# Kernel optimization log

Hardware: AMD Instinct MI355X
Metric: run time of the kernel (lower is better)

## Reference

```python
import jax, jax.numpy as jnp
import numpy as np
import math

EMB_DIM = 2048
HEAD_NUMS = 16
HEAD_DIM = EMB_DIM // HEAD_NUMS


def setup_inputs() -> dict:
    key = jax.random.key(0)
    k1, k2, k3, k4, k5 = jax.random.split(key, 5)
    B, S = 2, 2048
    X = jax.random.normal(k1, (B, S, EMB_DIM), dtype=jnp.float32)
    mask = jnp.ones((B, S), dtype=jnp.int32)
    # torch nn.Linear weights: [out_features, in_features]
    W_qkv = jax.random.normal(k2, (3 * EMB_DIM, EMB_DIM), dtype=jnp.float32) / math.sqrt(EMB_DIM)
    b_qkv = jax.random.normal(k3, (3 * EMB_DIM,), dtype=jnp.float32) * 0.01
    W_o = jax.random.normal(k4, (EMB_DIM, EMB_DIM), dtype=jnp.float32) / math.sqrt(EMB_DIM)
    b_o = jax.random.normal(k5, (EMB_DIM,), dtype=jnp.float32) * 0.01
    return {"X": X, "mask": mask, "W_qkv": W_qkv, "b_qkv": b_qkv, "W_o": W_o, "b_o": b_o}


def _rope_tables(seq_len):
    # Bug-faithful to source: exponent divides by full emb_dim, not head_dim.
    angle = 1.0 / jnp.power(10000.0, jnp.arange(0, HEAD_DIM, 2, dtype=jnp.float32) / EMB_DIM)
    t = jnp.arange(seq_len, dtype=jnp.float32)
    freqs = t[:, None] * angle[None, :]            # [S, HEAD_DIM//2]
    freqs = jnp.repeat(freqs, 2, axis=-1)          # [S, HEAD_DIM] (repeat_interleave)
    return jnp.cos(freqs), jnp.sin(freqs)


def _trans(x):
    # de-interleave pairs, then concat([-odd, even]) along last dim (as in source)
    B, H, S, D = x.shape
    xr = x.reshape(B, H, S, D // 2, 2)
    x1, x2 = xr[..., 0], xr[..., 1]
    return jnp.concatenate([-x2, x1], axis=-1)


def reference(X, mask, W_qkv, b_qkv, W_o, b_o):
    B, S, E = X.shape
    cos, sin = _rope_tables(S)                      # [S, HEAD_DIM]
    qkv = X @ W_qkv.T + b_qkv                       # [B, S, 3E]
    qkv = qkv.reshape(B, S, 3, HEAD_NUMS, HEAD_DIM).transpose(2, 0, 3, 1, 4)
    Q, K, V = qkv[0], qkv[1], qkv[2]                # [B, H, S, D]
    c = cos[None, None, :, :]
    s = sin[None, None, :, :]
    Q = c * Q + s * _trans(Q)
    K = c * K + s * _trans(K)
    scores = jnp.einsum('bhqd,bhkd->bhqk', Q, K) / math.sqrt(HEAD_DIM)
    pad = mask[:, None, None, :]                    # [B,1,1,S]
    scores = jnp.where(pad == 0, -1e9, scores)
    attn = jax.nn.softmax(scores, axis=-1)          # dropout = identity (eval)
    out = jnp.einsum('bhqk,bhkd->bhqd', attn, V)    # [B,H,S,D]
    out = out.transpose(0, 2, 1, 3).reshape(B, S, E)
    return out @ W_o.T + b_o
```

## Files before the change

### kernel.cpp

```cpp
#include <hip/hip_runtime.h>
#include <hip/hip_bf16.h>
#include <math.h>

typedef __bf16 bf16x8 __attribute__((ext_vector_type(8)));
typedef float  f32x4  __attribute__((ext_vector_type(4)));
typedef float  f32x16 __attribute__((ext_vector_type(16)));
typedef unsigned short ushort_t;
typedef ushort_t us4 __attribute__((ext_vector_type(4)));

#define MFMA16(a, b, c) __builtin_amdgcn_mfma_f32_16x16x32_bf16((a), (b), (c), 0, 0, 0)
#define MFMA32(a, b, c) __builtin_amdgcn_mfma_f32_32x32x16_bf16((a), (b), (c), 0, 0, 0)

__device__ __forceinline__ float bf2f(ushort_t h) {
    union { unsigned u; float f; } v; v.u = ((unsigned)h) << 16; return v.f;
}
__device__ __forceinline__ ushort_t f2bf(float x) {
    union { float f; unsigned u; } v; v.f = x;
    unsigned r = v.u + 0x7FFFu + ((v.u >> 16) & 1u);
    return (ushort_t)(r >> 16);
}
__device__ __forceinline__ void gl2lds16(const void* g, void* l) {
    __builtin_amdgcn_global_load_lds((__attribute__((address_space(1))) void*)(g),
                                     (__attribute__((address_space(3))) void*)(l),
                                     16, 0, 0);
}

__global__ __launch_bounds__(256) void detect_kernel(const ushort_t* __restrict__ w, int* flag)
{
    __shared__ int cnt[256];
    const int t = threadIdx.x;
    int c = 0;
    for (int i = t; i < 65536; i += 256) {
        const unsigned hw = w[i];
        const unsigned e = (hw >> 7) & 0xFFu;
        if (e == 0xFFu || (e == 0u && (hw & 0x7Fu) != 0u)) c++;
    }
    cnt[t] = c;
    __syncthreads();
    for (int s = 128; s > 0; s >>= 1) {
        if (t < s) cnt[t] += cnt[t + s];
        __syncthreads();
    }
    if (t == 0) flag[0] = (cnt[0] >= 8) ? 1 : 0;
}

__global__ __launch_bounds__(256) void convert_kernel(const void* __restrict__ src,
                                                      ushort_t* __restrict__ dst,
                                                      int n, const int* __restrict__ flag)
{
    const int i0 = (blockIdx.x * 256 + threadIdx.x) * 8;
    if (i0 + 8 > n) return;
    if (flag[0]) {
        const f32x4 a = *(const f32x4*)((const float*)src + i0);
        const f32x4 b = *(const f32x4*)((const float*)src + i0 + 4);
        ushort_t o[8];
        o[0]=f2bf(a[0]); o[1]=f2bf(a[1]); o[2]=f2bf(a[2]); o[3]=f2bf(a[3]);
        o[4]=f2bf(b[0]); o[5]=f2bf(b[1]); o[6]=f2bf(b[2]); o[7]=f2bf(b[3]);
        *(bf16x8*)(dst + i0) = *(const bf16x8*)o;
    } else {
        *(bf16x8*)(dst + i0) = *(const bf16x8*)((const ushort_t*)src + i0);
    }
}

__global__ __launch_bounds__(512, 2) void gemm256_bt_bias(
    const ushort_t* __restrict__ A, const ushort_t* __restrict__ B,
    const ushort_t* __restrict__ bias, ushort_t* __restrict__ C,
    int M, int N, int K)
{
    __shared__ __align__(16) ushort_t SM[65536];
    const int tid = threadIdx.x;
    const int l = tid & 63, ln = l & 15, q2 = l >> 4;
    const int w = tid >> 6, wm = w >> 2, wn = w & 3;
    const int m0 = blockIdx.y * 256, n0 = blockIdx.x * 256;
    const int NT = K >> 6;

#define STG_A256(slot, kbase, o) do { \
    const int s_ = (o) * 512 + tid; const int r_ = s_ >> 2; \
    const int q_ = (s_ & 3) ^ ((r_ >> 1) & 3); \
    gl2lds16(A + (size_t)(m0 + r_) * K + (kbase) + q_ * 8, \
             SM + (slot) * 16384 + s_ * 8); } while (0)
#define STG_B256(slot, kbase, o) do { \
    const int s_ = (o) * 512 + tid; const int r_ = s_ >> 2; \
    const int q_ = (s_ & 3) ^ ((r_ >> 1) & 3); \
    gl2lds16(B + (size_t)(n0 + r_) * K + (kbase) + q_ * 8, \
             SM + (slot) * 16384 + 8192 + s_ * 8); } while (0)
#define DSA256(slot, row) (*(const bf16x8*)(SM + (slot) * 16384 + (row) * 32 + ((q2 ^ (((row) >> 1) & 3)) << 3)))
#define DSB256(slot, row) (*(const bf16x8*)(SM + (slot) * 16384 + 8192 + (row) * 32 + ((q2 ^ (((row) >> 1) & 3)) << 3)))
#define BAR256() asm volatile("s_barrier" ::: "memory")

    f32x4 acc[8][4];
    const f32x4 z4 = {0.f, 0.f, 0.f, 0.f};
#pragma unroll
    for (int i = 0; i < 8; i++)
#pragma unroll
        for (int j = 0; j < 4; j++) acc[i][j] = z4;

    STG_A256(0, 0, 0);  STG_A256(0, 0, 1);  STG_B256(0, 0, 0);  STG_B256(0, 0, 1);
    STG_A256(1, 32, 0); STG_A256(1, 32, 1); STG_B256(1, 32, 0); STG_B256(1, 32, 1);
    if (NT > 1) STG_A256(2, 64, 0);
    asm volatile("s_waitcnt vmcnt(5)" ::: "memory");
    BAR256();

    for (int t = 0; t < NT; ++t) {
        const int s0 = (2 * t) & 3, s1 = (2 * t + 1) & 3;
        const int sA = (2 * t + 2) & 3, sB = (2 * t + 3) & 3;
        const int kA = (t + 1) << 6, kB = kA + 32, kC = (t + 2) << 6;
        const bool stAB = (t < NT - 1), stC = (t < NT - 2);
        const int rA0 = wm * 128, rA1 = wm * 128 + 64, rB = wn * 64;
        bf16x8 a0[4], a1[4], b00[2], b01[2], b10[2], b11[2];

#pragma unroll
        for (int ii = 0; ii < 4; ii++) a0[ii] = DSA256(s0, rA0 + ii * 16 + ln);
        b00[0] = DSB256(s0, rB + ln);
        b00[1] = DSB256(s0, rB + 16 + ln);
        if (stAB) STG_A256(sA, kA, 1);
        __builtin_amdgcn_s_setprio(1);
#pragma unroll
        for (int ii = 0; ii < 4; ii++) {
            acc[ii][0] = MFMA16(a0[ii], b00[0], acc[ii][0]);
            acc[ii][1] = MFMA16(a0[ii], b00[1], acc[ii][1]);
        }
        __builtin_amdgcn_s_setprio(0);
        if (stAB) { asm volatile("s_waitcnt vmcnt(2)" ::: "memory"); }
        else      { asm volatile("s_waitcnt vmcnt(0)" ::: "memory"); }
        BAR256();

#pragma unroll
        for (int ii = 0; ii < 4; ii++) a1[ii] = DSA256(s1, rA0 + ii * 16 + ln);
        b01[0] = DSB256(s1, rB + ln);
        b01[1] = DSB256(s1, rB + 16 + ln);
        if (stAB) STG_B256(sA, kA, 0);
        __builtin_amdgcn_s_setprio(1);
#pragma unroll
        for (int ii = 0; ii < 4; ii++) {
            acc[ii][0] = MFMA16(a1[ii], b01[0], acc[ii][0]);
            acc[ii][1] = MFMA16(a1[ii], b01[1], acc[ii][1]);
        }
        __builtin_amdgcn_s_setprio(0);
        BAR256();

        b10[0] = DSB256(s0, rB + 32 + ln);
        b10[1] = DSB256(s0, rB + 48 + ln);
        if (stAB) STG_B256(sA, kA, 1);
        __builtin_amdgcn_s_setprio(1);
#pragma unroll
        for (int ii = 0; ii < 4; ii++) {
            acc[ii][2] = MFMA16(a0[ii], b10[0], acc[ii][2]);
            acc[ii][3] = MFMA16(a0[ii], b10[1], acc[ii][3]);
        }
        __builtin_amdgcn_s_setprio(0);
        BAR256();

        b11[0] = DSB256(s1, rB + 32 + ln);
        b11[1] = DSB256(s1, rB + 48 + ln);
        if (stAB) STG_A256(sB, kB, 0);
        __builtin_amdgcn_s_setprio(1);
#pragma unroll
        for (int ii = 0; ii < 4; ii++) {
            acc[ii][2] = MFMA16(a1[ii], b11[0], acc[ii][2]);
            acc[ii][3] = MFMA16(a1[ii], b11[1], acc[ii][3]);
        }
        __builtin_amdgcn_s_setprio(0);
        BAR256();

#pragma unroll
        for (int ii = 0; ii < 4; ii++) a0[ii] = DSA256(s0, rA1 + ii * 16 + ln);
        if (stAB) STG_A256(sB, kB, 1);
        __builtin_amdgcn_s_setprio(1);
#pragma unroll
        for (int ii = 0; ii < 4; ii++) {
            acc[4 + ii][2] = MFMA16(a0[ii], b10[0], acc[4 + ii][2]);
            acc[4 + ii][3] = MFMA16(a0[ii], b10[1], acc[4 + ii][3]);
        }
        __builtin_amdgcn_s_setprio(0);
        BAR256();

#pragma unroll
        for (int ii = 0; ii < 4; ii++) a1[ii] = DSA256(s1, rA1 + ii * 16 + ln);
        if (stAB) STG_B256(sB, kB, 0);
        __builtin_amdgcn_s_setprio(1);
#pragma unroll
        for (int ii = 0; ii < 4; ii++) {
            acc[4 + ii][2] = MFMA16(a1[ii], b11[0], acc[4 + ii][2]);
            acc[4 + ii][3] = MFMA16(a1[ii], b11[1], acc[4 + ii][3]);
        }
        __builtin_amdgcn_s_setprio(0);
        BAR256();

        if (stAB) STG_B256(sB, kB, 1);
        __builtin_amdgcn_s_setprio(1);
#pragma unroll
        for (int ii = 0; ii < 4; ii++) {
            acc[4 + ii][0] = MFMA16(a0[ii], b00[0], acc[4 + ii][0]);
            acc[4 + ii][1] = MFMA16(a0[ii], b00[1], acc[4 + ii][1]);
        }
        __builtin_amdgcn_s_setprio(0);
        BAR256();

        if (stC) STG_A256(s0, kC, 0);
        __builtin_amdgcn_s_setprio(1);
#pragma unroll
        for (int ii = 0; ii < 4; ii++) {
            acc[4 + ii][0] = MFMA16(a1[ii], b01[0], acc[4 + ii][0]);
            acc[4 + ii][1] = MFMA16(a1[ii], b01[1], acc[4 + ii][1]);
        }
        __builtin_amdgcn_s_setprio(0);
        if (t < NT - 2)       { asm volatile("s_waitcnt vmcnt(5)" ::: "memory"); }
        else if (t == NT - 2) { asm volatile("s_waitcnt vmcnt(4)" ::: "memory"); }
        BAR256();
    }

#pragma unroll
    for (int j = 0; j < 4; j++) {
        const int n = n0 + wn * 64 + j * 16 + ln;
        const float bv = bf2f(bias[n]);
#pragma unroll
        for (int i = 0; i < 8; i++) {
            const int mrow = m0 + wm * 128 + i * 16 + q2 * 4;
#pragma unroll
            for (int r = 0; r < 4; r++)
                C[(size_t)(mrow + r) * N + n] = f2bf(acc[i][j][r] + bv);
        }
    }
#undef STG_A256
#undef STG_B256
#undef DSA256
#undef DSB256
#undef BAR256
}

__global__ __launch_bounds__(256) void gemm_bt_bias_out(
    const ushort_t* __restrict__ A, const ushort_t* __restrict__ B,
    const ushort_t* __restrict__ bias, void* __restrict__ C,
    int M, int N, int K, const int* __restrict__ flag)
{
    __shared__ __align__(16) ushort_t As[128 * 32];
    __shared__ __align__(16) ushort_t Bs[128 * 32];
    const int tid = threadIdx.x;
    const int w = tid >> 6, l = tid & 63, q = l >> 4, ln = l & 15;
    const int wm = w >> 1, wn = w & 1;
    const int m0 = blockIdx.y * 128, n0 = blockIdx.x * 128;
    const int sr = tid >> 2;
    const int sc = (tid & 3) * 8;

    f32x4 acc[4][4];
    const f32x4 z4 = {0.f, 0.f, 0.f, 0.f};
    for (int i = 0; i < 4; i++) for (int j = 0; j < 4; j++) acc[i][j] = z4;

    for (int k0 = 0; k0 < K; k0 += 32) {
        __syncthreads();
        gl2lds16(A + (size_t)(m0 + sr) * K + k0 + sc,       As + sr * 32 + sc);
        gl2lds16(A + (size_t)(m0 + 64 + sr) * K + k0 + sc,  As + (64 + sr) * 32 + sc);
        gl2lds16(B + (size_t)(n0 + sr) * K + k0 + sc,       Bs + sr * 32 + sc);
        gl2lds16(B + (size_t)(n0 + 64 + sr) * K + k0 + sc,  Bs + (64 + sr) * 32 + sc);
        __syncthreads();
        bf16x8 a[4], bb[4];
        for (int i = 0; i < 4; i++)
            a[i]  = *(const bf16x8*)(As + (wm * 64 + i * 16 + ln) * 32 + q * 8);
        for (int j = 0; j < 4; j++)
            bb[j] = *(const bf16x8*)(Bs + (wn * 64 + j * 16 + ln) * 32 + q * 8);
        for (int i = 0; i < 4; i++)
            for (int j = 0; j < 4; j++)
                acc[i][j] = MFMA16(a[i], bb[j], acc[i][j]);
    }
    const int f = flag[0];
    for (int j = 0; j < 4; j++) {
        const int n = n0 + wn * 64 + j * 16 + ln;
        const float bv = bf2f(bias[n]);
        for (int i = 0; i < 4; i++) {
            const int mrow = m0 + wm * 64 + i * 16 + q * 4;
            for (int r = 0; r < 4; r++) {
                const float val = acc[i][j][r] + bv;
                const size_t idx = (size_t)(mrow + r) * N + n;
                if (f) ((float*)C)[idx] = val;
                else   ((ushort_t*)C)[idx] = f2bf(val);
            }
        }
    }
}

__global__ __launch_bounds__(256) void rope_kernel(ushort_t* qkv)
{
    const int bs = blockIdx.x;
    const int s = bs & 2047;
    const int t = threadIdx.x;
    const size_t base = (size_t)bs * 6144;
    float cv[8], sv[8], qa[8], qp[8], ka[8], kp[8];
    for (int u = 0; u < 8; u++) {
        const int e = u * 256 + t;
        const int j = e & 127;
        const int p = (j < 64) ? (2 * j + 1) : (2 * (j - 64));
        const int hb = e - j;
        const float ang = powf(10000.0f, -(float)(2 * (j >> 1)) / 2048.0f);
        sincosf((float)s * ang, &sv[u], &cv[u]);
        qa[u] = bf2f(qkv[base + hb + j]);
        qp[u] = bf2f(qkv[base + hb + p]);
        ka[u] = bf2f(qkv[base + 2048 + hb + j]);
        kp[u] = bf2f(qkv[base + 2048 + hb + p]);
    }
    __syncthreads();
    for (int u = 0; u < 8; u++) {
        const int e = u * 256 + t;
        const int j = e & 127;
        const int hb = e - j;
        const float sg = (j < 64) ? -1.0f : 1.0f;
        qkv[base + hb + j]        = f2bf(cv[u] * qa[u] + sv[u] * sg * qp[u]);
        qkv[base + 2048 + hb + j] = f2bf(cv[u] * ka[u] + sv[u] * sg * kp[u]);
    }
}

__global__ __launch_bounds__(256) void vtrans_kernel(const ushort_t* __restrict__ qkv,
                                                     ushort_t* __restrict__ Vt)
{
    __shared__ ushort_t tile[64][130];
    const int blk = blockIdx.x;
    const int st = blk & 31, h = (blk >> 5) & 15, b = blk >> 9;
    const int t = threadIdx.x;
    for (int i = 0; i < 32; i++) {
        const int e = i * 256 + t;
        const int r = e >> 7, c = e & 127;
        tile[r][c] = qkv[(size_t)(b * 2048 + st * 64 + r) * 6144 + 4096 + h * 128 + c];
    }
    __syncthreads();
    const int d = t >> 1, s0 = (t & 1) * 32;
    const size_t obase = ((size_t)(b * 16 + h) * 128 + d) * 2048 + st * 64 + s0;
    for (int k = 0; k < 32; k++)
        Vt[obase + k] = tile[s0 + k][d];
}

__global__ __launch_bounds__(256, 2) void flash_kernel(
    const ushort_t* __restrict__ qkv, const ushort_t* __restrict__ Vt,
    const int* __restrict__ mask, ushort_t* __restrict__ AO)
{
    __shared__ __align__(16) ushort_t SM[16384];
    ushort_t* Ks = SM;
    ushort_t* Vs = SM + 8192;
    const int t = threadIdx.x;
    const int w = t >> 6, l = t & 63, lq = l & 31, q2 = l >> 5;
    const int qb = blockIdx.x * 128, h = blockIdx.y, b = blockIdx.z;
    const size_t brow = (size_t)b * 2048;
    const float scale = 0.08838834764831845f;
    const int qrow = qb + w * 32 + lq;
    const size_t vbase = (size_t)(b * 16 + h) * 128;

    bf16x8 qf[8];
#pragma unroll
    for (int kb = 0; kb < 8; kb++)
        qf[kb] = *(const bf16x8*)(qkv + (brow + qrow) * 6144 + h * 128 + kb * 16 + q2 * 8);

    float m_old = -1e30f, lsum = 0.f;
    f32x16 acc_o[4];
#pragma unroll
    for (int dt = 0; dt < 4; dt++)
#pragma unroll
        for (int r = 0; r < 16; r++) acc_o[dt][r] = 0.f;

    bf16x8 kst[4], vst[4];
#pragma unroll
    for (int i = 0; i < 4; i++) {
        const int s_ = i * 256 + t; const int row = s_ >> 4; const int u = s_ & 15;
        kst[i] = *(const bf16x8*)(qkv + (brow + row) * 6144 + 2048 + h * 128 + u * 8);
    }
#pragma unroll
    for (int i = 0; i < 4; i++) {
        const int s_ = i * 256 + t; const int row = s_ >> 3; const int u = s_ & 7;
        vst[i] = *(const bf16x8*)(Vt + (vbase + row) * 2048 + u * 8);
    }

    for (int s0 = 0; s0 < 2048; s0 += 64) {
        const int mk = mask[brow + s0 + l];
        const unsigned long long bm = __ballot(mk != 0);
        asm volatile("s_waitcnt lgkmcnt(0)" ::: "memory");
        asm volatile("s_barrier" ::: "memory");
#pragma unroll
        for (int i = 0; i < 4; i++) {
            const int s_ = i * 256 + t; const int row = s_ >> 4; const int u = s_ & 15;
            *(bf16x8*)(Ks + row * 128 + ((u ^ (row & 15)) << 3)) = kst[i];
        }
#pragma unroll
        for (int i = 0; i < 4; i++) {
            const int s_ = i * 256 + t; const int row = s_ >> 3; const int u = s_ & 7;
            *(bf16x8*)(Vs + row * 64 + ((u ^ (row & 7)) << 3)) = vst[i];
        }
        if (s0 + 64 < 2048) {
#pragma unroll
            for (int i = 0; i < 4; i++) {
                const int s_ = i * 256 + t; const int row = s_ >> 4; const int u = s_ & 15;
                kst[i] = *(const bf16x8*)(qkv + (brow + s0 + 64 + row) * 6144 + 2048 + h * 128 + u * 8);
            }
#pragma unroll
            for (int i = 0; i < 4; i++) {
                const int s_ = i * 256 + t; const int row = s_ >> 3; const int u = s_ & 7;
                vst[i] = *(const bf16x8*)(Vt + (vbase + row) * 2048 + s0 + 64 + u * 8);
            }
        }
        asm volatile("s_waitcnt lgkmcnt(0)" ::: "memory");
        asm volatile("s_barrier" ::: "memory");

        f32x16 sa[2];
#pragma unroll
        for (int mt = 0; mt < 2; mt++) {
#pragma unroll
            for (int r = 0; r < 16; r++) sa[mt][r] = 0.f;
            const int row = mt * 32 + lq;
            __builtin_amdgcn_s_setprio(1);
#pragma unroll
            for (int kb = 0; kb < 8; kb++) {
                bf16x8 a = *(const bf16x8*)(Ks + row * 128 + (((kb * 2 + q2) ^ (row & 15)) << 3));
                sa[mt] = MFMA32(a, qf[kb], sa[mt]);
            }
            __builtin_amdgcn_s_setprio(0);
        }
        float p[32];
        float mr = -1e30f;
        if (bm == ~0ull) {
#pragma unroll
            for (int mt = 0; mt < 2; mt++)
#pragma unroll
                for (int r = 0; r < 16; r++) {
                    const float v = sa[mt][r] * scale;
                    p[mt * 16 + r] = v;
                    mr = fmaxf(mr, v);
                }
        } else {
#pragma unroll
            for (int mt = 0; mt < 2; mt++)
#pragma unroll
                for (int r = 0; r < 16; r++) {
                    const int srow = mt * 32 + (r & 3) + 8 * (r >> 2) + 4 * q2;
                    const float bias = ((bm >> srow) & 1ull) ? 0.f : -1e9f;
                    const float v = sa[mt][r] * scale + bias;
                    p[mt * 16 + r] = v;
                    mr = fmaxf(mr, v);
                }
        }
        mr = fmaxf(mr, __shfl_xor(mr, 32, 64));
        if (!__all(mr <= m_old + 8.0f)) {
            const float mnew = fmaxf(m_old, mr);
            const float alpha = __expf(m_old - mnew);
            lsum *= alpha;
#pragma unroll
            for (int dt = 0; dt < 4; dt++)
#pragma unroll
                for (int r = 0; r < 16; r++) acc_o[dt][r] *= alpha;
            m_old = mnew;
        }
        float rs = 0.f;
#pragma unroll
        for (int i = 0; i < 32; i++) { p[i] = __expf(p[i] - m_old); rs += p[i]; }
        rs += __shfl_xor(rs, 32, 64);
        lsum += rs;

#pragma unroll
        for (int kb = 0; kb < 4; kb++) {
            const int bb = (kb >> 1) * 16 + (kb & 1) * 8;
            unsigned w01, w23, w45, w67;
            asm("v_cvt_pk_bf16_f32 %0, %1, %2" : "=v"(w01) : "v"(p[bb + 0]), "v"(p[bb + 1]));
            asm("v_cvt_pk_bf16_f32 %0, %1, %2" : "=v"(w23) : "v"(p[bb + 2]), "v"(p[bb + 3]));
            asm("v_cvt_pk_bf16_f32 %0, %1, %2" : "=v"(w45) : "v"(p[bb + 4]), "v"(p[bb + 5]));
            asm("v_cvt_pk_bf16_f32 %0, %1, %2" : "=v"(w67) : "v"(p[bb + 6]), "v"(p[bb + 7]));
            asm("v_permlane32_swap_b32 %0, %1" : "+v"(w01), "+v"(w45));
            asm("v_permlane32_swap_b32 %0, %1" : "+v"(w23), "+v"(w67));
            union { unsigned u[4]; bf16x8 v8; } pu;
            pu.u[0] = w01; pu.u[1] = w23; pu.u[2] = w45; pu.u[3] = w67;
            __builtin_amdgcn_s_setprio(1);
#pragma unroll
            for (int dt = 0; dt < 4; dt++) {
                const int row = dt * 32 + lq;
                bf16x8 va = *(const bf16x8*)(Vs + row * 64 + (((kb * 2 + q2) ^ (row & 7)) << 3));
                acc_o[dt] = MFMA32(va, pu.v8, acc_o[dt]);
            }
            __builtin_amdgcn_s_setprio(0);
        }
    }
    __syncthreads();
    const float inv = (lsum > 0.f) ? 1.0f / lsum : 0.f;
#pragma unroll
    for (int dt = 0; dt < 4; dt++)
#pragma unroll
        for (int r2 = 0; r2 < 4; r2++) {
            us4 ov;
#pragma unroll
            for (int j = 0; j < 4; j++) ov[j] = f2bf(acc_o[dt][r2 * 4 + j] * inv);
            const int row = w * 32 + lq;
            const int unit = dt * 4 + r2;
            *(us4*)(SM + row * 128 + ((unit ^ (row & 15)) << 3) + q2 * 4) = ov;
        }
    __syncthreads();
#pragma unroll
    for (int i = 0; i < 8; i++) {
        const int rl = i * 4 + (l >> 4), ch = l & 15;
        const int row = w * 32 + rl;
        bf16x8 vv = *(const bf16x8*)(SM + row * 128 + ((ch ^ (row & 15)) << 3));
        *(bf16x8*)(AO + (brow + qb + row) * 2048 + h * 128 + ch * 8) = vv;
    }
}

extern "C" void kernel_launch(void* const* d_in, const int* in_sizes, int n_in,
                              void* d_out, int out_size, void* d_ws, size_t ws_size,
                              hipStream_t stream)
{
    (void)in_sizes; (void)n_in; (void)out_size; (void)ws_size;
    const void* X    = d_in[0];
    const int*  mask = (const int*)d_in[1];
    const void* Wqkv = d_in[2];
    const void* bqkv = d_in[3];
    const void* Wo   = d_in[4];
    const void* bo   = d_in[5];

    int*      flag  = (int*)d_ws;
    ushort_t* Xc    = (ushort_t*)d_ws + 16;
    ushort_t* Wqkvc = Xc + 8388608;
    ushort_t* bqkvc = Wqkvc + 12582912;
    ushort_t* Woc   = bqkvc + 6144;
    ushort_t* boc   = Woc + 4194304;
    ushort_t* qkv   = boc + 2048;
    ushort_t* Vt    = Wqkvc;
    ushort_t* AO    = Xc;

    detect_kernel<<<1, 256, 0, stream>>>((const ushort_t*)Wqkv, flag);
    convert_kernel<<<4096, 256, 0, stream>>>(X,    Xc,    8388608,  flag);
    convert_kernel<<<6144, 256, 0, stream>>>(Wqkv, Wqkvc, 12582912, flag);
    convert_kernel<<<3,    256, 0, stream>>>(bqkv, bqkvc, 6144,     flag);
    convert_kernel<<<2048, 256, 0, stream>>>(Wo,   Woc,   4194304,  flag);
    convert_kernel<<<1,    256, 0, stream>>>(bo,   boc,   2048,     flag);

    gemm256_bt_bias<<<dim3(6144 / 256, 4096 / 256), 512, 0, stream>>>(Xc, Wqkvc, bqkvc, qkv, 4096, 6144, 2048);
    rope_kernel<<<4096, 256, 0, stream>>>(qkv);
    vtrans_kernel<<<1024, 256, 0, stream>>>(qkv, Vt);
    flash_kernel<<<dim3(16, 16, 2), 256, 0, stream>>>(qkv, Vt, mask, AO);
    gemm_bt_bias_out<<<dim3(2048 / 128, 4096 / 128), 256, 0, stream>>>(AO, Woc, boc, d_out, 4096, 2048, 2048, flag);
}
```

Baseline: 578.9 us.

## Restructure 256-tile GEMM main loop into four phases with larger MFMA bursts

Replaces the eight-phase ping-pong schedule, each phase issuing 8 MFMAs, with four phases of 16 MFMAs each. All four B fragments per k-half are now held in registers. Global-to-LDS stages are issued in pairs, and the early prefetch of the third k-slab is dropped. The aim is to halve the number of workgroup barriers per iteration and give the matrix unit longer uninterrupted bursts, at the cost of more live registers and less lead time on prefetches. The vmcnt wait counts are adjusted to the new issue pattern, and any mismatch there could cause LDS read hazards.

```diff
diff --git a/kernel.cpp b/kernel.cpp
--- a/kernel.cpp
+++ b/kernel.cpp
@@ -97,116 +97,70 @@
 
     STG_A256(0, 0, 0);  STG_A256(0, 0, 1);  STG_B256(0, 0, 0);  STG_B256(0, 0, 1);
     STG_A256(1, 32, 0); STG_A256(1, 32, 1); STG_B256(1, 32, 0); STG_B256(1, 32, 1);
-    if (NT > 1) STG_A256(2, 64, 0);
-    asm volatile("s_waitcnt vmcnt(5)" ::: "memory");
+    asm volatile("s_waitcnt vmcnt(4)" ::: "memory");
     BAR256();
 
     for (int t = 0; t < NT; ++t) {
         const int s0 = (2 * t) & 3, s1 = (2 * t + 1) & 3;
         const int sA = (2 * t + 2) & 3, sB = (2 * t + 3) & 3;
-        const int kA = (t + 1) << 6, kB = kA + 32, kC = (t + 2) << 6;
-        const bool stAB = (t < NT - 1), stC = (t < NT - 2);
+        const int kA = (t + 1) << 6, kB = kA + 32;
+        const bool stAB = (t < NT - 1);
         const int rA0 = wm * 128, rA1 = wm * 128 + 64, rB = wn * 64;
-        bf16x8 a0[4], a1[4], b00[2], b01[2], b10[2], b11[2];
-
-#pragma unroll
-        for (int ii = 0; ii < 4; ii++) a0[ii] = DSA256(s0, rA0 + ii * 16 + ln);
-        b00[0] = DSB256(s0, rB + ln);
-        b00[1] = DSB256(s0, rB + 16 + ln);
-        if (stAB) STG_A256(sA, kA, 1);
+        bf16x8 a[4], b0[4], b1[4];
+
+#pragma unroll
+        for (int ii = 0; ii < 4; ii++) a[ii]  = DSA256(s0, rA0 + ii * 16 + ln);
+#pragma unroll
+        for (int jj = 0; jj < 4; jj++) b0[jj] = DSB256(s0, rB + jj * 16 + ln);
+        if (stAB) { STG_A256(sA, kA, 0); STG_A256(sA, kA, 1); }
         __builtin_amdgcn_s_setprio(1);
 #pragma unroll
-        for (int ii = 0; ii < 4; ii++) {
-            acc[ii][0] = MFMA16(a0[ii], b00[0], acc[ii][0]);
-            acc[ii][1] = MFMA16(a0[ii], b00[1], acc[ii][1]);
-        }
+        for (int ii = 0; ii < 4; ii++)
+#pragma unroll
+            for (int jj = 0; jj < 4; jj++)
+                acc[ii][jj] = MFMA16(a[ii], b0[jj], acc[ii][jj]);
         __builtin_amdgcn_s_setprio(0);
         if (stAB) { asm volatile("s_waitcnt vmcnt(2)" ::: "memory"); }
         else      { asm volatile("s_waitcnt vmcnt(0)" ::: "memory"); }
         BAR256();
 
 #pragma unroll
-        for (int ii = 0; ii < 4; ii++) a1[ii] = DSA256(s1, rA0 + ii * 16 + ln);
-        b01[0] = DSB256(s1, rB + ln);
-        b01[1] = DSB256(s1, rB + 16 + ln);
-        if (stAB) STG_B256(sA, kA, 0);
+        for (int ii = 0; ii < 4; ii++) a[ii]  = DSA256(s1, rA0 + ii * 16 + ln);
+#pragma unroll
+        for (int jj = 0; jj < 4; jj++) b1[jj] = DSB256(s1, rB + jj * 16 + ln);
+        if (stAB) { STG_B256(sA, kA, 0); STG_B256(sA, kA, 1); }
         __builtin_amdgcn_s_setprio(1);
 #pragma unroll
-        for (int ii = 0; ii < 4; ii++) {
-            acc[ii][0] = MFMA16(a1[ii], b01[0], acc[ii][0]);
-            acc[ii][1] = MFMA16(a1[ii], b01[1], acc[ii][1]);
-        }
+        for (int ii = 0; ii < 4; ii++)
+#pragma unroll
+            for (int jj = 0; jj < 4; jj++)
+                acc[ii][jj] = MFMA16(a[ii], b1[jj], acc[ii][jj]);
         __builtin_amdgcn_s_setprio(0);
         BAR256();
 
-        b10[0] = DSB256(s0, rB + 32 + ln);
-        b10[1] = DSB256(s0, rB + 48 + ln);
-        if (stAB) STG_B256(sA, kA, 1);
+#pragma unroll
+        for (int ii = 0; ii < 4; ii++) a[ii] = DSA256(s0, rA1 + ii * 16 + ln);
+        if (stAB) { STG_A256(sB, kB, 0); STG_A256(sB, kB, 1); }
         __builtin_amdgcn_s_setprio(1);
 #pragma unroll
-        for (int ii = 0; ii < 4; ii++) {
-            acc[ii][2] = MFMA16(a0[ii], b10[0], acc[ii][2]);
-            acc[ii][3] = MFMA16(a0[ii], b10[1], acc[ii][3]);
-        }
+        for (int ii = 0; ii < 4; ii++)
+#pragma unroll
+            for (int jj = 0; jj < 4; jj++)
+                acc[4 + ii][jj] = MFMA16(a[ii], b0[jj], acc[4 + ii][jj]);
         __builtin_amdgcn_s_setprio(0);
         BAR256();
 
-        b11[0] = DSB256(s1, rB + 32 + ln);
-        b11[1] = DSB256(s1, rB + 48 + ln);
-        if (stAB) STG_A256(sB, kB, 0);
+#pragma unroll
+        for (int ii = 0; ii < 4; ii++) a[ii] = DSA256(s1, rA1 + ii * 16 + ln);
+        if (stAB) { STG_B256(sB, kB, 0); STG_B256(sB, kB, 1); }
         __builtin_amdgcn_s_setprio(1);
 #pragma unroll
-        for (int ii = 0; ii < 4; ii++) {
-            acc[ii][2] = MFMA16(a1[ii], b11[0], acc[ii][2]);
-            acc[ii][3] = MFMA16(a1[ii], b11[1], acc[ii][3]);
-        }
+        for (int ii = 0; ii < 4; ii++)
+#pragma unroll
+            for (int jj = 0; jj < 4; jj++)
+                acc[4 + ii][jj] = MFMA16(a[ii], b1[jj], acc[4 + ii][jj]);
         __builtin_amdgcn_s_setprio(0);
-        BAR256();
-
-#pragma unroll
-        for (int ii = 0; ii < 4; ii++) a0[ii] = DSA256(s0, rA1 + ii * 16 + ln);
-        if (stAB) STG_A256(sB, kB, 1);
-        __builtin_amdgcn_s_setprio(1);
-#pragma unroll
-        for (int ii = 0; ii < 4; ii++) {
-            acc[4 + ii][2] = MFMA16(a0[ii], b10[0], acc[4 + ii][2]);
-            acc[4 + ii][3] = MFMA16(a0[ii], b10[1], acc[4 + ii][3]);
-        }
-        __builtin_amdgcn_s_setprio(0);
-        BAR256();
-
-#pragma unroll
-        for (int ii = 0; ii < 4; ii++) a1[ii] = DSA256(s1, rA1 + ii * 16 + ln);
-        if (stAB) STG_B256(sB, kB, 0);
-        __builtin_amdgcn_s_setprio(1);
-#pragma unroll
-        for (int ii = 0; ii < 4; ii++) {
-            acc[4 + ii][2] = MFMA16(a1[ii], b11[0], acc[4 + ii][2]);
-            acc[4 + ii][3] = MFMA16(a1[ii], b11[1], acc[4 + ii][3]);
-        }
-        __builtin_amdgcn_s_setprio(0);
-        BAR256();
-
-        if (stAB) STG_B256(sB, kB, 1);
-        __builtin_amdgcn_s_setprio(1);
-#pragma unroll
-        for (int ii = 0; ii < 4; ii++) {
-            acc[4 + ii][0] = MFMA16(a0[ii], b00[0], acc[4 + ii][0]);
-            acc[4 + ii][1] = MFMA16(a0[ii], b00[1], acc[4 + ii][1]);
-        }
-        __builtin_amdgcn_s_setprio(0);
-        BAR256();
-
-        if (stC) STG_A256(s0, kC, 0);
-        __builtin_amdgcn_s_setprio(1);
-#pragma unroll
-        for (int ii = 0; ii < 4; ii++) {
-            acc[4 + ii][0] = MFMA16(a1[ii], b01[0], acc[4 + ii][0]);
-            acc[4 + ii][1] = MFMA16(a1[ii], b01[1], acc[4 + ii][1]);
-        }
-        __builtin_amdgcn_s_setprio(0);
-        if (t < NT - 2)       { asm volatile("s_waitcnt vmcnt(5)" ::: "memory"); }
-        else if (t == NT - 2) { asm volatile("s_waitcnt vmcnt(4)" ::: "memory"); }
+        if (stAB) { asm volatile("s_waitcnt vmcnt(4)" ::: "memory"); }
         BAR256();
     }
 
```

New measurement: 579.0 us. Within noise of the previous version (+0.0%).
